# Kernel tuning notes

Measured on AMD Instinct MI355X. Metric: run time of the kernel, lower is better.

## Reference

```python
import jax, jax.numpy as jnp
import numpy as np
import math

DIM = 384
HEADS = 6
HEAD_DIM = DIM // HEADS
MLP_HIDDEN = int(DIM * 2.0)


def layer_norm(x, g, b, eps=1e-5):
    mu = jnp.mean(x, axis=-1, keepdims=True)
    var = jnp.mean((x - mu) ** 2, axis=-1, keepdims=True)
    return (x - mu) * jax.lax.rsqrt(var + eps) * g + b


def setup_inputs() -> dict:
    key = jax.random.key(0)
    ks = jax.random.split(key, 12)
    B, N = 4, 2048
    s = 0.02
    return {
        "x": jax.random.normal(ks[0], (B, N, DIM), dtype=jnp.float32),
        "pos": jax.random.normal(ks[1], (B, N, 3), dtype=jnp.float32),
        "qkv_w": jax.random.normal(ks[2], (DIM, 3 * DIM), dtype=jnp.float32) * s,
        "qkv_b": jnp.zeros((3 * DIM,), jnp.float32),
        "proj_w": jax.random.normal(ks[3], (DIM, DIM), dtype=jnp.float32) * s,
        "proj_b": jnp.zeros((DIM,), jnp.float32),
        "mlp_w1": jax.random.normal(ks[4], (DIM, MLP_HIDDEN), dtype=jnp.float32) * s,
        "mlp_b1": jnp.zeros((MLP_HIDDEN,), jnp.float32),
        "mlp_w2": jax.random.normal(ks[5], (MLP_HIDDEN, DIM), dtype=jnp.float32) * s,
        "mlp_b2": jnp.zeros((DIM,), jnp.float32),
        "ln1_g": jnp.ones((DIM,), jnp.float32),
        "ln1_b": jnp.zeros((DIM,), jnp.float32),
        "ln2_g": jnp.ones((DIM,), jnp.float32),
        "ln2_b": jnp.zeros((DIM,), jnp.float32),
    }


def reference(x, pos, qkv_w, qkv_b, proj_w, proj_b, mlp_w1, mlp_b1,
              mlp_w2, mlp_b2, ln1_g, ln1_b, ln2_g, ln2_b):
    B, N, D = x.shape
    H, Hd = HEADS, HEAD_DIM
    # qkv projection
    qkv = layer_norm(x, ln1_g, ln1_b) @ qkv_w + qkv_b          # [B,N,3D]
    qkv = qkv.reshape(B, N, 3, H, Hd)
    q = jnp.transpose(qkv[:, :, 0], (0, 2, 1, 3))               # [B,H,N,Hd]
    k = jnp.transpose(qkv[:, :, 1], (0, 2, 1, 3))
    v = jnp.transpose(qkv[:, :, 2], (0, 2, 1, 3))
    # pairwise squared-distance bias: exp(-||p_i - p_j||^2)
    rel = pos[:, :, None, :] - pos[:, None, :, :]               # [B,N,N,3]
    dist = jnp.exp(-jnp.sum(rel ** 2, axis=-1))                 # [B,N,N]
    scale = 1.0 / math.sqrt(Hd)
    attn = jnp.einsum('bhqd,bhkd->bhqk', q, k) * scale + dist[:, None, :, :]
    attn = jax.nn.softmax(attn, axis=-1)
    out = jnp.einsum('bhqk,bhkd->bhqd', attn, v)                # [B,H,N,Hd]
    out = jnp.transpose(out, (0, 2, 1, 3)).reshape(B, N, D)
    out = out @ proj_w + proj_b
    x = x + out
    h = layer_norm(x, ln2_g, ln2_b)
    h = jax.nn.gelu(h @ mlp_w1 + mlp_b1, approximate=False) @ mlp_w2 + mlp_b2
    return x + h
```

## Files before the change

kernel.cpp:

```cpp
#include <hip/hip_runtime.h>
#include <hip/hip_bf16.h>
#include <math.h>

#define DIMD 384
#define NHEADS 6
#define HD 64
#define MLPH 768
#define SEQ 2048
#define NBATCH 4
#define NTOK (NBATCH*SEQ)

typedef __hip_bfloat16 bf16;

typedef __attribute__((ext_vector_type(8))) short bf16x8;
typedef __attribute__((ext_vector_type(4))) float f32x4;

#define LOG2E 1.44269504088896340736f

static __device__ inline float fexp2(float x) { return __builtin_amdgcn_exp2f(x); }

static __device__ inline f32x4 mfma16(bf16x8 a, bf16x8 b, f32x4 c) {
    return __builtin_amdgcn_mfma_f32_16x16x32_bf16(a, b, c, 0, 0, 0);
}

static __device__ inline unsigned int cvtpk(float lo, float hi) {
    unsigned int r;
    asm("v_cvt_pk_bf16_f32 %0, %1, %2" : "=v"(r) : "v"(lo), "v"(hi));
    return r;
}
static __device__ inline float bflo(unsigned int u) { return __builtin_bit_cast(float, u << 16); }
static __device__ inline float bfhi(unsigned int u) { return __builtin_bit_cast(float, u & 0xffff0000u); }

static __device__ inline void gld16(const void* g, void* l) {
    __builtin_amdgcn_global_load_lds(
        (const __attribute__((address_space(1))) unsigned int*)g,
        (__attribute__((address_space(3))) unsigned int*)l, 16, 0, 0);
}

__global__ __launch_bounds__(256) void ln_k(const float* __restrict__ x,
                                            const float* __restrict__ gm,
                                            const float* __restrict__ bt,
                                            bf16* __restrict__ out) {
    int row = blockIdx.x * 4 + (threadIdx.x >> 6);
    int l = threadIdx.x & 63;
    const float* xr = x + (size_t)row * DIMD;
    float v[6];
#pragma unroll
    for (int j = 0; j < 6; ++j) v[j] = xr[l + 64 * j];
    float s = 0.f, s2 = 0.f;
#pragma unroll
    for (int j = 0; j < 6; ++j) { s += v[j]; s2 += v[j] * v[j]; }
#pragma unroll
    for (int m = 1; m < 64; m <<= 1) { s += __shfl_xor(s, m); s2 += __shfl_xor(s2, m); }
    float mu = s * (1.f / DIMD);
    float var = s2 * (1.f / DIMD) - mu * mu;
    float rs = rsqrtf(var + 1e-5f);
    bf16* orow = out + (size_t)row * DIMD;
#pragma unroll
    for (int j = 0; j < 6; ++j) {
        int i = l + 64 * j;
        orow[i] = __float2bfloat16((v[j] - mu) * rs * gm[i] + bt[i]);
    }
}

__global__ __launch_bounds__(256) void prep_k(const float* __restrict__ w1,
                                              const float* __restrict__ w2,
                                              const float* __restrict__ w3,
                                              const float* __restrict__ w4,
                                              bf16* __restrict__ o1,
                                              bf16* __restrict__ o2,
                                              bf16* __restrict__ o3,
                                              bf16* __restrict__ o4,
                                              const float* __restrict__ pos,
                                              bf16* __restrict__ DP,
                                              const float* __restrict__ x,
                                              const float* __restrict__ g1,
                                              const float* __restrict__ b1,
                                              bf16* __restrict__ xn) {
    __shared__ float t[32][33];
    int id = blockIdx.x;
    if (id < 1152) {
        const float* W; bf16* O; int K, N;
        if (id < 432)      { W = w1; O = o1; K = 384; N = 1152; }
        else if (id < 576) { W = w2; O = o2; K = 384; N = 384;  id -= 432; }
        else if (id < 864) { W = w3; O = o3; K = 384; N = 768;  id -= 576; }
        else               { W = w4; O = o4; K = 768; N = 384;  id -= 864; }
        int nbx = N >> 5;
        int nb = (id % nbx) * 32, kb = (id / nbx) * 32;
        int tx = threadIdx.x & 31, ty = threadIdx.x >> 5;
#pragma unroll
        for (int i = 0; i < 4; ++i)
            t[ty + 8 * i][tx] = W[(size_t)(kb + ty + 8 * i) * N + nb + tx];
        __syncthreads();
#pragma unroll
        for (int i = 0; i < 4; ++i)
            O[(size_t)(nb + ty + 8 * i) * K + kb + tx] = __float2bfloat16(t[tx][ty + 8 * i]);
    } else if (id < 1664) {
        int blk = id - 1152;
        int w = blk & 3, qt = (blk >> 2) & 31, b = blk >> 7;
        int l = threadIdx.x & 63, tt = threadIdx.x >> 6;
        int lq = l & 15, g = l >> 4;
        int q = qt * 64 + w * 16 + lq;
        const float* pq = pos + ((size_t)b * SEQ + q) * 3;
        float px = pq[0], py = pq[1], pz = pq[2];
        const float* posb = pos + (size_t)b * SEQ * 3;
        char* base = (char*)DP + (size_t)blk * 65536;
        for (int j = 0; j < 8; ++j) {
            int tt8 = tt * 8 + j;
#pragma unroll
            for (int m = 0; m < 2; ++m) {
                int k0 = tt8 * 64 + 32 * m + 4 * g;
                float a[24];
                const float* pk = posb + 3 * k0;
                *(f32x4*)&a[0]  = *(const f32x4*)pk;
                *(f32x4*)&a[4]  = *(const f32x4*)(pk + 4);
                *(f32x4*)&a[8]  = *(const f32x4*)(pk + 8);
                const float* pk2 = posb + 3 * (k0 + 16);
                *(f32x4*)&a[12] = *(const f32x4*)pk2;
                *(f32x4*)&a[16] = *(const f32x4*)(pk2 + 4);
                *(f32x4*)&a[20] = *(const f32x4*)(pk2 + 8);
                float o8[8];
#pragma unroll
                for (int r = 0; r < 8; ++r) {
                    float dx = px - a[3 * r], dy = py - a[3 * r + 1], dz = pz - a[3 * r + 2];
                    o8[r] = fexp2(-LOG2E * (dx * dx + dy * dy + dz * dz)) * LOG2E;
                }
                uint4 o;
                o.x = cvtpk(o8[0], o8[1]); o.y = cvtpk(o8[2], o8[3]);
                o.z = cvtpk(o8[4], o8[5]); o.w = cvtpk(o8[6], o8[7]);
                *(uint4*)(base + ((size_t)tt8 * 2 + m) * 1024 + l * 16) = o;
            }
        }
    } else {
        int row = (id - 1664) * 4 + (threadIdx.x >> 6);
        int l = threadIdx.x & 63;
        const float* xr = x + (size_t)row * DIMD;
        float v[6];
#pragma unroll
        for (int j = 0; j < 6; ++j) v[j] = xr[l + 64 * j];
        float s = 0.f, s2 = 0.f;
#pragma unroll
        for (int j = 0; j < 6; ++j) { s += v[j]; s2 += v[j] * v[j]; }
#pragma unroll
        for (int m = 1; m < 64; m <<= 1) { s += __shfl_xor(s, m); s2 += __shfl_xor(s2, m); }
        float mu = s * (1.f / DIMD);
        float var = s2 * (1.f / DIMD) - mu * mu;
        float rs = rsqrtf(var + 1e-5f);
        bf16* orow = xn + (size_t)row * DIMD;
#pragma unroll
        for (int j = 0; j < 6; ++j) {
            int i = l + 64 * j;
            orow[i] = __float2bfloat16((v[j] - mu) * rs * g1[i] + b1[i]);
        }
    }
}

template <int EPI>
__global__ __launch_bounds__(256) void gemm128_k(const bf16* __restrict__ A,
                                                 const bf16* __restrict__ WT,
                                                 const float* __restrict__ bias,
                                                 bf16* __restrict__ ob0,
                                                 bf16* __restrict__ ob1,
                                                 bf16* __restrict__ ob2,
                                                 int K, int Nw) {
    __shared__ __align__(16) char Als[2][8192];
    __shared__ __align__(16) char Bls[2][8192];
    int tid = threadIdx.x;
    int w = tid >> 6, l = tid & 63;
    int c = l & 15, g = l >> 4;
    int wr = w >> 1, wc = w & 1;
    int m0 = blockIdx.y * 128, n0 = blockIdx.x * 128;
    const char* Ag = (const char*)A + (size_t)m0 * K * 2;
    const char* Bg = (const char*)WT + (size_t)n0 * K * 2;
    int K2 = K * 2;

    f32x4 acc[4][4];
#pragma unroll
    for (int mi = 0; mi < 4; ++mi)
#pragma unroll
        for (int ni = 0; ni < 4; ++ni) acc[mi][ni] = (f32x4){0.f, 0.f, 0.f, 0.f};

    auto stage = [&](int t, int bi) {
#pragma unroll
        for (int p = 0; p < 2; ++p) {
            int chunk = p * 256 + tid;
            int r = chunk >> 2;
            int cc = ((chunk & 3) ^ (r & 3)) << 4;
            gld16(Ag + (size_t)r * K2 + t * 64 + cc, &Als[bi][chunk * 16]);
            gld16(Bg + (size_t)r * K2 + t * 64 + cc, &Bls[bi][chunk * 16]);
        }
    };

    stage(0, 0);
    int kcn = K >> 5;
    for (int t = 0; t < kcn; ++t) {
        int bi = t & 1;
        __syncthreads();
        if (t + 1 < kcn) stage(t + 1, bi ^ 1);
        bf16x8 af[4], bfr[4];
#pragma unroll
        for (int mi = 0; mi < 4; ++mi) {
            int row = wr * 64 + mi * 16 + c;
            __builtin_memcpy(&af[mi], &Als[bi][row * 64 + ((g ^ (row & 3)) << 4)], 16);
        }
#pragma unroll
        for (int ni = 0; ni < 4; ++ni) {
            int row = wc * 64 + ni * 16 + c;
            __builtin_memcpy(&bfr[ni], &Bls[bi][row * 64 + ((g ^ (row & 3)) << 4)], 16);
        }
#pragma unroll
        for (int mi = 0; mi < 4; ++mi)
#pragma unroll
            for (int ni = 0; ni < 4; ++ni)
                acc[mi][ni] = mfma16(af[mi], bfr[ni], acc[mi][ni]);
    }

#pragma unroll
    for (int mi = 0; mi < 4; ++mi) {
#pragma unroll
        for (int ni = 0; ni < 4; ++ni) {
            int ntb = n0 + wc * 64 + ni * 16;
#pragma unroll
            for (int r = 0; r < 4; ++r) {
                int m = m0 + wr * 64 + mi * 16 + 4 * g + r;
                int n = ntb + c;
                float val = acc[mi][ni][r] + bias[n];
                if (EPI == 0) {
                    int which = ntb / DIMD;
                    int rem = ntb - which * DIMD;
                    int h = rem >> 6;
                    int d = (rem & 63) + c;
                    int b = m >> 11, s = m & (SEQ - 1);
                    if (which == 2) {
                        int slot = (s & ~31) + 8 * ((m & 15) >> 2) + 4 * ((m >> 4) & 1) + (m & 3);
                        ob2[(((size_t)b * NHEADS + h) * HD + d) * SEQ + slot] = __float2bfloat16(val);
                    } else {
                        bf16* dp = which == 0 ? ob0 : ob1;
                        dp[(((size_t)b * NHEADS + h) * SEQ + s) * HD + d] = __float2bfloat16(val);
                    }
                } else {
                    float ge = 0.5f * val * (1.0f + erff(val * 0.70710678118654752f));
                    ob0[(size_t)m * Nw + n] = __float2bfloat16(ge);
                }
            }
        }
    }
}

__global__ __launch_bounds__(256) void gemm_k(const bf16* __restrict__ A,
                                              const bf16* __restrict__ WT,
                                              const float* __restrict__ bias,
                                              const float* __restrict__ resid,
                                              float* __restrict__ outf,
                                              int K, int Nw) {
    __shared__ __align__(16) char Als[2][8192];
    __shared__ __align__(16) char Bls[2][8192];
    int tid = threadIdx.x;
    int w = tid >> 6, l = tid & 63;
    int c = l & 15, g = l >> 4;
    int m0 = blockIdx.y * 64, n0 = blockIdx.x * 64;
    const char* Ag = (const char*)A + (size_t)m0 * K * 2;
    const char* Bg = (const char*)WT + (size_t)n0 * K * 2;
    int K2 = K * 2;

    f32x4 acc[4];
#pragma unroll
    for (int nt = 0; nt < 4; ++nt) acc[nt] = (f32x4){0.f, 0.f, 0.f, 0.f};

    auto stage = [&](int t, int bi) {
#pragma unroll
        for (int p = 0; p < 2; ++p) {
            int chunk = p * 256 + tid;
            int r = chunk >> 3;
            int cc = ((chunk & 7) ^ (r & 7)) << 4;
            gld16(Ag + (size_t)r * K2 + t * 128 + cc, &Als[bi][chunk * 16]);
            gld16(Bg + (size_t)r * K2 + t * 128 + cc, &Bls[bi][chunk * 16]);
        }
    };

    stage(0, 0);
    int kcn = K >> 6;
    int arow = (16 * w + c) * 128;
    int sw = c & 7;
    for (int t = 0; t < kcn; ++t) {
        int bi = t & 1;
        __syncthreads();
        if (t + 1 < kcn) stage(t + 1, bi ^ 1);
#pragma unroll
        for (int kk = 0; kk < 2; ++kk) {
            int ch = ((kk * 4 + g) ^ sw) << 4;
            bf16x8 af;
            __builtin_memcpy(&af, &Als[bi][arow + ch], 16);
#pragma unroll
            for (int nt = 0; nt < 4; ++nt) {
                bf16x8 bfr;
                __builtin_memcpy(&bfr, &Bls[bi][(nt * 16 + c) * 128 + ch], 16);
                acc[nt] = mfma16(af, bfr, acc[nt]);
            }
        }
    }

#pragma unroll
    for (int nt = 0; nt < 4; ++nt) {
        int ntb = n0 + nt * 16;
#pragma unroll
        for (int r = 0; r < 4; ++r) {
            int m = m0 + 16 * w + 4 * g + r;
            int n = ntb + c;
            float val = acc[nt][r] + bias[n];
            val += resid[(size_t)m * Nw + n];
            outf[(size_t)m * Nw + n] = val;
        }
    }
}

__global__ __launch_bounds__(256) void attn_k(const bf16* __restrict__ q,
                                              const bf16* __restrict__ k,
                                              const bf16* __restrict__ vT,
                                              const bf16* __restrict__ DP,
                                              bf16* __restrict__ out) {
    __shared__ __align__(16) char Kls[3][8192];
    __shared__ __align__(16) char Vls[3][8192];

    int tid = threadIdx.x;
    int w = tid >> 6, l = tid & 63;
    int lq = l & 15, g = l >> 4;
    int qt = blockIdx.x & 31;
    int bh = blockIdx.x >> 5;
    int b = bh / NHEADS, h = bh % NHEADS;
    int qrow = qt * 64 + w * 16 + lq;

    const bf16* qp = q + ((size_t)bh * SEQ + qrow) * HD + 8 * g;
    bf16x8 qf0 = *(const bf16x8*)qp;
    bf16x8 qf1 = *(const bf16x8*)(qp + 32);

    const char* kgb = (const char*)(k + (size_t)bh * SEQ * HD);
    const char* vgb = (const char*)(vT + (size_t)bh * HD * SEQ);
    const char* dpb = (const char*)DP + ((size_t)((b * 32 + qt) * 4 + w)) * 65536 + l * 16;

    const float SC2 = 0.125f * LOG2E;
    f32x4 oacc[4];
#pragma unroll
    for (int dt = 0; dt < 4; ++dt) oacc[dt] = (f32x4){0.f, 0.f, 0.f, 0.f};
    f32x4 osum = (f32x4){0.f, 0.f, 0.f, 0.f};
    bf16x8 ones = {(short)0x3F80, (short)0x3F80, (short)0x3F80, (short)0x3F80,
                   (short)0x3F80, (short)0x3F80, (short)0x3F80, (short)0x3F80};

    int swq = lq & 7;
    int offA = lq * 128 + ((g ^ swq) << 4);
    int offB = lq * 128 + (((4 + g) ^ swq) << 4);

    auto stage = [&](int t, int B2) {
#pragma unroll
        for (int p = 0; p < 2; ++p) {
            int chunk = p * 256 + tid;
            int r = chunk >> 3, c = chunk & 7;
            int cc = (c ^ (r & 7)) << 4;
            gld16(kgb + (size_t)t * 8192 + r * 128 + cc, &Kls[B2][chunk * 16]);
            gld16(vgb + (size_t)r * 4096 + t * 128 + cc, &Vls[B2][chunk * 16]);
        }
    };

    stage(0, 0);
    uint4 cdp0 = *(const uint4*)(dpb);
    uint4 cdp1 = *(const uint4*)(dpb + 1024);
    stage(1, 1);

    auto body = [&](int t, int B0, int B2) {
        asm volatile("s_waitcnt vmcnt(4)" ::: "memory");
        __builtin_amdgcn_sched_barrier(0);
        __builtin_amdgcn_s_barrier();
        __builtin_amdgcn_sched_barrier(0);

        const char* Kb = &Kls[B0][0];
        const char* Vb = &Vls[B0][0];
        f32x4 st[4];
        __builtin_amdgcn_s_setprio(1);
#pragma unroll
        for (int s = 0; s < 4; ++s) {
            bf16x8 klo, khi;
            __builtin_memcpy(&klo, Kb + s * 2048 + offA, 16);
            __builtin_memcpy(&khi, Kb + s * 2048 + offB, 16);
            f32x4 z = (f32x4){0.f, 0.f, 0.f, 0.f};
            st[s] = mfma16(klo, qf0, z);
            st[s] = mfma16(khi, qf1, st[s]);
        }
        __builtin_amdgcn_s_setprio(0);

#pragma unroll
        for (int m = 0; m < 2; ++m) {
            uint4 cd = m == 0 ? cdp0 : cdp1;
            int offV = m == 0 ? offA : offB;
            f32x4 s0v = st[2 * m], s1v = st[2 * m + 1];
            float p[8];
            p[0] = fexp2(s0v[0] * SC2 + bflo(cd.x));
            p[1] = fexp2(s0v[1] * SC2 + bfhi(cd.x));
            p[2] = fexp2(s0v[2] * SC2 + bflo(cd.y));
            p[3] = fexp2(s0v[3] * SC2 + bfhi(cd.y));
            p[4] = fexp2(s1v[0] * SC2 + bflo(cd.z));
            p[5] = fexp2(s1v[1] * SC2 + bfhi(cd.z));
            p[6] = fexp2(s1v[2] * SC2 + bflo(cd.w));
            p[7] = fexp2(s1v[3] * SC2 + bfhi(cd.w));

            unsigned int pw[4];
            pw[0] = cvtpk(p[0], p[1]);
            pw[1] = cvtpk(p[2], p[3]);
            pw[2] = cvtpk(p[4], p[5]);
            pw[3] = cvtpk(p[6], p[7]);
            bf16x8 pf;
            __builtin_memcpy(&pf, pw, 16);

            __builtin_amdgcn_s_setprio(1);
            osum = mfma16(ones, pf, osum);
#pragma unroll
            for (int dt = 0; dt < 4; ++dt) {
                bf16x8 vf;
                __builtin_memcpy(&vf, Vb + dt * 2048 + offV, 16);
                oacc[dt] = mfma16(vf, pf, oacc[dt]);
            }
            __builtin_amdgcn_s_setprio(0);
        }

        __builtin_amdgcn_sched_barrier(0);
        int tn1 = t + 1 < 32 ? t + 1 : 31;
        const char* dpn = dpb + (size_t)tn1 * 2048;
        uint4 n0 = *(const uint4*)(dpn);
        uint4 n1 = *(const uint4*)(dpn + 1024);
        __builtin_amdgcn_sched_barrier(0);
        int tn2 = t + 2 < 32 ? t + 2 : 31;
        stage(tn2, B2);
        __builtin_amdgcn_sched_barrier(0);
        cdp0 = n0; cdp1 = n1;
    };

    for (int t = 0; t < 30; t += 3) {
        body(t + 0, 0, 2);
        body(t + 1, 1, 0);
        body(t + 2, 2, 1);
    }
    body(30, 0, 2);
    body(31, 1, 0);

    float inv = 1.f / osum[0];
    bf16* op = out + ((size_t)b * SEQ + qrow) * DIMD + h * HD + 4 * g;
#pragma unroll
    for (int dt = 0; dt < 4; ++dt) {
        unsigned int t2[2];
        t2[0] = cvtpk(oacc[dt][0] * inv, oacc[dt][1] * inv);
        t2[1] = cvtpk(oacc[dt][2] * inv, oacc[dt][3] * inv);
        __builtin_memcpy(op + dt * 16, t2, 8);
    }
}

extern "C" void kernel_launch(void* const* d_in, const int* in_sizes, int n_in,
                              void* d_out, int out_size, void* d_ws, size_t ws_size,
                              hipStream_t stream) {
    const float* x      = (const float*)d_in[0];
    const float* pos    = (const float*)d_in[1];
    const float* qkv_w  = (const float*)d_in[2];
    const float* qkv_b  = (const float*)d_in[3];
    const float* proj_w = (const float*)d_in[4];
    const float* proj_b = (const float*)d_in[5];
    const float* mlp_w1 = (const float*)d_in[6];
    const float* mlp_b1 = (const float*)d_in[7];
    const float* mlp_w2 = (const float*)d_in[8];
    const float* mlp_b2 = (const float*)d_in[9];
    const float* ln1_g  = (const float*)d_in[10];
    const float* ln1_b  = (const float*)d_in[11];
    const float* ln2_g  = (const float*)d_in[12];
    const float* ln2_b  = (const float*)d_in[13];

    char* p = (char*)d_ws;
    size_t off = 0;
    auto alloc = [&](size_t bytes) {
        char* r = p + off;
        off = (off + bytes + 255) & ~(size_t)255;
        return r;
    };
    bf16* WT1 = (bf16*)alloc((size_t)1152 * 384 * 2);
    bf16* WT2 = (bf16*)alloc((size_t)384 * 384 * 2);
    bf16* WT3 = (bf16*)alloc((size_t)384 * 768 * 2);
    bf16* WT4 = (bf16*)alloc((size_t)768 * 384 * 2);
    bf16* xn  = (bf16*)alloc((size_t)NTOK * DIMD * 2);
    bf16* xn2 = (bf16*)alloc((size_t)NTOK * DIMD * 2);
    bf16* qb  = (bf16*)alloc((size_t)NTOK * DIMD * 2);
    bf16* kb  = (bf16*)alloc((size_t)NTOK * DIMD * 2);
    bf16* vTb = (bf16*)alloc((size_t)NTOK * DIMD * 2);
    bf16* ao  = (bf16*)alloc((size_t)NTOK * DIMD * 2);
    float* x1 = (float*)alloc((size_t)NTOK * DIMD * 4);
    bf16* hh  = (bf16*)alloc((size_t)NTOK * MLPH * 2);
    bf16* dtab = (bf16*)alloc((size_t)NBATCH * SEQ * SEQ * 2);
    if (off > ws_size) return;

    prep_k<<<1152 + 512 + 2048, 256, 0, stream>>>(
        qkv_w, proj_w, mlp_w1, mlp_w2, WT1, WT2, WT3, WT4,
        pos, dtab, x, ln1_g, ln1_b, xn);

    gemm128_k<0><<<dim3(1152 / 128, NTOK / 128), 256, 0, stream>>>(
        xn, WT1, qkv_b, qb, kb, vTb, 384, 1152);
    attn_k<<<NBATCH * NHEADS * (SEQ / 64), 256, 0, stream>>>(qb, kb, vTb, dtab, ao);
    gemm_k<<<dim3(384 / 64, NTOK / 64), 256, 0, stream>>>(
        ao, WT2, proj_b, x, x1, 384, 384);
    ln_k<<<NTOK / 4, 256, 0, stream>>>(x1, ln2_g, ln2_b, xn2);
    gemm128_k<2><<<dim3(768 / 128, NTOK / 128), 256, 0, stream>>>(
        xn2, WT3, mlp_b1, hh, nullptr, nullptr, 384, 768);
    gemm_k<<<dim3(384 / 64, NTOK / 64), 256, 0, stream>>>(
        hh, WT4, mlp_b2, x1, (float*)d_out, 768, 384);
}
```

Baseline: 139.8 us.

## Compute distance bias in attention via MFMA with split-bf16 position features

Replaces the precomputed 32MB bf16 pairwise distance-bias table with per-token feature vectors (hi/lo bf16 splits of pos, -2*pos and squared norm). The attention kernel now gets ||p_i-p_j||^2 from one extra MFMA per 16x16 tile and applies the exp inside the loop. This removes the large table write in prep and its reread in attention. In exchange it adds an extra exp2 per score and more VALU work, and the split-bf16 expansion may lose some precision.

```diff
diff --git a/kernel.cpp b/kernel.cpp
--- a/kernel.cpp
+++ b/kernel.cpp
@@ -30,6 +30,13 @@
 }
 static __device__ inline float bflo(unsigned int u) { return __builtin_bit_cast(float, u << 16); }
 static __device__ inline float bfhi(unsigned int u) { return __builtin_bit_cast(float, u & 0xffff0000u); }
+
+static __device__ inline unsigned short bfb(float f) {
+    return __builtin_bit_cast(unsigned short, __float2bfloat16(f));
+}
+static __device__ inline float bf2f(unsigned short u) {
+    return __builtin_bit_cast(float, (unsigned int)u << 16);
+}
 
 static __device__ inline void gld16(const void* g, void* l) {
     __builtin_amdgcn_global_load_lds(
@@ -72,7 +79,8 @@
                                               bf16* __restrict__ o3,
                                               bf16* __restrict__ o4,
                                               const float* __restrict__ pos,
-                                              bf16* __restrict__ DP,
+                                              unsigned short* __restrict__ PA,
+                                              unsigned short* __restrict__ PB,
                                               const float* __restrict__ x,
                                               const float* __restrict__ g1,
                                               const float* __restrict__ b1,
@@ -95,44 +103,27 @@
 #pragma unroll
         for (int i = 0; i < 4; ++i)
             O[(size_t)(nb + ty + 8 * i) * K + kb + tx] = __float2bfloat16(t[tx][ty + 8 * i]);
-    } else if (id < 1664) {
-        int blk = id - 1152;
-        int w = blk & 3, qt = (blk >> 2) & 31, b = blk >> 7;
-        int l = threadIdx.x & 63, tt = threadIdx.x >> 6;
-        int lq = l & 15, g = l >> 4;
-        int q = qt * 64 + w * 16 + lq;
-        const float* pq = pos + ((size_t)b * SEQ + q) * 3;
-        float px = pq[0], py = pq[1], pz = pq[2];
-        const float* posb = pos + (size_t)b * SEQ * 3;
-        char* base = (char*)DP + (size_t)blk * 65536;
-        for (int j = 0; j < 8; ++j) {
-            int tt8 = tt * 8 + j;
-#pragma unroll
-            for (int m = 0; m < 2; ++m) {
-                int k0 = tt8 * 64 + 32 * m + 4 * g;
-                float a[24];
-                const float* pk = posb + 3 * k0;
-                *(f32x4*)&a[0]  = *(const f32x4*)pk;
-                *(f32x4*)&a[4]  = *(const f32x4*)(pk + 4);
-                *(f32x4*)&a[8]  = *(const f32x4*)(pk + 8);
-                const float* pk2 = posb + 3 * (k0 + 16);
-                *(f32x4*)&a[12] = *(const f32x4*)pk2;
-                *(f32x4*)&a[16] = *(const f32x4*)(pk2 + 4);
-                *(f32x4*)&a[20] = *(const f32x4*)(pk2 + 8);
-                float o8[8];
-#pragma unroll
-                for (int r = 0; r < 8; ++r) {
-                    float dx = px - a[3 * r], dy = py - a[3 * r + 1], dz = pz - a[3 * r + 2];
-                    o8[r] = fexp2(-LOG2E * (dx * dx + dy * dy + dz * dz)) * LOG2E;
-                }
-                uint4 o;
-                o.x = cvtpk(o8[0], o8[1]); o.y = cvtpk(o8[2], o8[3]);
-                o.z = cvtpk(o8[4], o8[5]); o.w = cvtpk(o8[6], o8[7]);
-                *(uint4*)(base + ((size_t)tt8 * 2 + m) * 1024 + l * 16) = o;
-            }
-        }
+    } else if (id < 1184) {
+        int i = (id - 1152) * 256 + threadIdx.x;
+        const float* pp = pos + (size_t)i * 3;
+        float px = pp[0], py = pp[1], pz = pp[2];
+        float n2 = px * px + py * py + pz * pz;
+        unsigned short xh = bfb(px), yh = bfb(py), zh = bfb(pz);
+        unsigned short xl = bfb(px - bf2f(xh)), yl = bfb(py - bf2f(yh)), zl = bfb(pz - bf2f(zh));
+        unsigned short nh = bfb(n2);
+        unsigned short nl = bfb(n2 - bf2f(nh));
+        float ux = -2.f * px, uy = -2.f * py, uz = -2.f * pz;
+        unsigned short uxh = bfb(ux), uyh = bfb(uy), uzh = bfb(uz);
+        unsigned short uxl = bfb(ux - bf2f(uxh)), uyl = bfb(uy - bf2f(uyh)), uzl = bfb(uz - bf2f(uzh));
+        const unsigned short ONE = 0x3F80;
+        unsigned short A[16] = {xh, xh, xl, yh, yh, yl, zh, zh, zl, nh, nl, ONE, ONE, 0, 0, 0};
+        unsigned short B[16] = {uxh, uxl, uxh, uyh, uyl, uyh, uzh, uzl, uzh, ONE, ONE, nh, nl, 0, 0, 0};
+        *(uint4*)(PA + (size_t)i * 16)     = *(uint4*)&A[0];
+        *(uint4*)(PA + (size_t)i * 16 + 8) = *(uint4*)&A[8];
+        *(uint4*)(PB + (size_t)i * 16)     = *(uint4*)&B[0];
+        *(uint4*)(PB + (size_t)i * 16 + 8) = *(uint4*)&B[8];
     } else {
-        int row = (id - 1664) * 4 + (threadIdx.x >> 6);
+        int row = (id - 1184) * 4 + (threadIdx.x >> 6);
         int l = threadIdx.x & 63;
         const float* xr = x + (size_t)row * DIMD;
         float v[6];
@@ -317,7 +308,8 @@
 __global__ __launch_bounds__(256) void attn_k(const bf16* __restrict__ q,
                                               const bf16* __restrict__ k,
                                               const bf16* __restrict__ vT,
-                                              const bf16* __restrict__ DP,
+                                              const unsigned short* __restrict__ PA,
+                                              const unsigned short* __restrict__ PB,
                                               bf16* __restrict__ out) {
     __shared__ __align__(16) char Kls[3][8192];
     __shared__ __align__(16) char Vls[3][8192];
@@ -336,7 +328,11 @@
 
     const char* kgb = (const char*)(k + (size_t)bh * SEQ * HD);
     const char* vgb = (const char*)(vT + (size_t)bh * HD * SEQ);
-    const char* dpb = (const char*)DP + ((size_t)((b * 32 + qt) * 4 + w)) * 65536 + l * 16;
+    const char* pab = (const char*)(PA + (size_t)b * SEQ * 16);
+
+    bf16x8 pqf = {0, 0, 0, 0, 0, 0, 0, 0};
+    if (g < 2)
+        __builtin_memcpy(&pqf, (const char*)(PB + ((size_t)b * SEQ + qrow) * 16) + g * 16, 16);
 
     const float SC2 = 0.125f * LOG2E;
     f32x4 oacc[4];
@@ -361,46 +357,53 @@
         }
     };
 
+    auto loadPA = [&](int t, uint4* dst) {
+#pragma unroll
+        for (int s = 0; s < 4; ++s)
+            dst[s] = *(const uint4*)(pab + (size_t)(t * 64 + 16 * s + lq) * 32 + (g & 1) * 16);
+    };
+
     stage(0, 0);
-    uint4 cdp0 = *(const uint4*)(dpb);
-    uint4 cdp1 = *(const uint4*)(dpb + 1024);
+    uint4 cpa[4];
+    loadPA(0, cpa);
     stage(1, 1);
 
     auto body = [&](int t, int B0, int B2) {
-        asm volatile("s_waitcnt vmcnt(4)" ::: "memory");
+        asm volatile("s_waitcnt vmcnt(8)" ::: "memory");
         __builtin_amdgcn_sched_barrier(0);
         __builtin_amdgcn_s_barrier();
         __builtin_amdgcn_sched_barrier(0);
 
         const char* Kb = &Kls[B0][0];
         const char* Vb = &Vls[B0][0];
-        f32x4 st[4];
+        f32x4 st[4], d2[4];
         __builtin_amdgcn_s_setprio(1);
 #pragma unroll
         for (int s = 0; s < 4; ++s) {
-            bf16x8 klo, khi;
+            bf16x8 klo, khi, paf;
             __builtin_memcpy(&klo, Kb + s * 2048 + offA, 16);
             __builtin_memcpy(&khi, Kb + s * 2048 + offB, 16);
+            __builtin_memcpy(&paf, &cpa[s], 16);
             f32x4 z = (f32x4){0.f, 0.f, 0.f, 0.f};
             st[s] = mfma16(klo, qf0, z);
             st[s] = mfma16(khi, qf1, st[s]);
+            d2[s] = mfma16(paf, pqf, z);
         }
         __builtin_amdgcn_s_setprio(0);
 
 #pragma unroll
         for (int m = 0; m < 2; ++m) {
-            uint4 cd = m == 0 ? cdp0 : cdp1;
             int offV = m == 0 ? offA : offB;
             f32x4 s0v = st[2 * m], s1v = st[2 * m + 1];
+            f32x4 e0 = d2[2 * m], e1 = d2[2 * m + 1];
             float p[8];
-            p[0] = fexp2(s0v[0] * SC2 + bflo(cd.x));
-            p[1] = fexp2(s0v[1] * SC2 + bfhi(cd.x));
-            p[2] = fexp2(s0v[2] * SC2 + bflo(cd.y));
-            p[3] = fexp2(s0v[3] * SC2 + bfhi(cd.y));
-            p[4] = fexp2(s1v[0] * SC2 + bflo(cd.z));
-            p[5] = fexp2(s1v[1] * SC2 + bfhi(cd.z));
-            p[6] = fexp2(s1v[2] * SC2 + bflo(cd.w));
-            p[7] = fexp2(s1v[3] * SC2 + bfhi(cd.w));
+#pragma unroll
+            for (int i = 0; i < 4; ++i) {
+                float bias0 = fexp2(-LOG2E * e0[i]);
+                p[i] = fexp2(s0v[i] * SC2 + LOG2E * bias0);
+                float bias1 = fexp2(-LOG2E * e1[i]);
+                p[4 + i] = fexp2(s1v[i] * SC2 + LOG2E * bias1);
+            }
 
             unsigned int pw[4];
             pw[0] = cvtpk(p[0], p[1]);
@@ -423,14 +426,13 @@
 
         __builtin_amdgcn_sched_barrier(0);
         int tn1 = t + 1 < 32 ? t + 1 : 31;
-        const char* dpn = dpb + (size_t)tn1 * 2048;
-        uint4 n0 = *(const uint4*)(dpn);
-        uint4 n1 = *(const uint4*)(dpn + 1024);
+        uint4 npa[4];
+        loadPA(tn1, npa);
         __builtin_amdgcn_sched_barrier(0);
         int tn2 = t + 2 < 32 ? t + 2 : 31;
         stage(tn2, B2);
         __builtin_amdgcn_sched_barrier(0);
-        cdp0 = n0; cdp1 = n1;
+        cpa[0] = npa[0]; cpa[1] = npa[1]; cpa[2] = npa[2]; cpa[3] = npa[3];
     };
 
     for (int t = 0; t < 30; t += 3) {
@@ -489,16 +491,17 @@
     bf16* ao  = (bf16*)alloc((size_t)NTOK * DIMD * 2);
     float* x1 = (float*)alloc((size_t)NTOK * DIMD * 4);
     bf16* hh  = (bf16*)alloc((size_t)NTOK * MLPH * 2);
-    bf16* dtab = (bf16*)alloc((size_t)NBATCH * SEQ * SEQ * 2);
+    unsigned short* PA = (unsigned short*)alloc((size_t)NTOK * 16 * 2);
+    unsigned short* PB = (unsigned short*)alloc((size_t)NTOK * 16 * 2);
     if (off > ws_size) return;
 
-    prep_k<<<1152 + 512 + 2048, 256, 0, stream>>>(
+    prep_k<<<1152 + 32 + 2048, 256, 0, stream>>>(
         qkv_w, proj_w, mlp_w1, mlp_w2, WT1, WT2, WT3, WT4,
-        pos, dtab, x, ln1_g, ln1_b, xn);
+        pos, PA, PB, x, ln1_g, ln1_b, xn);
 
     gemm128_k<0><<<dim3(1152 / 128, NTOK / 128), 256, 0, stream>>>(
         xn, WT1, qkv_b, qb, kb, vTb, 384, 1152);
-    attn_k<<<NBATCH * NHEADS * (SEQ / 64), 256, 0, stream>>>(qb, kb, vTb, dtab, ao);
+    attn_k<<<NBATCH * NHEADS * (SEQ / 64), 256, 0, stream>>>(qb, kb, vTb, PA, PB, ao);
     gemm_k<<<dim3(384 / 64, NTOK / 64), 256, 0, stream>>>(
         ao, WT2, proj_b, x, x1, 384, 384);
     ln_k<<<NTOK / 4, 256, 0, stream>>>(x1, ln2_g, ln2_b, xn2);
```

Result: slower. 143.3 us (+2.5%).
